# Optimization experiments

Measured on AMD Instinct MI355X. Metric: run time of the kernel, lower is better.

Reference implementation:

```python
import jax, jax.numpy as jnp
import numpy as np


def setup_inputs() -> dict:
    key = jax.random.key(0)
    ks = jax.random.split(key, 5)
    b, t, q_dim, kv_dim, h = 16, 128, 256, 64, 4
    c = t - 1
    q_x = jax.random.normal(ks[0], (b, t, q_dim), dtype=jnp.float32)
    kv_x = jax.random.normal(ks[1], (b, t, c, kv_dim), dtype=jnp.float32)
    # Linear weights stored as [in, out]; no biases (bias=False in torch module).
    sq = 1.0 / np.sqrt(q_dim)
    sk = 1.0 / np.sqrt(kv_dim)
    Wq = jax.random.uniform(ks[2], (q_dim, kv_dim * h), jnp.float32, -sq, sq)
    Wk = jax.random.uniform(ks[3], (kv_dim, kv_dim * h), jnp.float32, -sk, sk)
    Wv = jax.random.uniform(ks[4], (kv_dim, kv_dim * h), jnp.float32, -sk, sk)
    return {"q_x": q_x, "kv_x": kv_x, "Wq": Wq, "Wk": Wk, "Wv": Wv}


def reference(q_x, kv_x, Wq, Wk, Wv):
    b, t, c, k = kv_x.shape  # c = t - 1
    h = Wq.shape[1] // k
    # projections
    q = (q_x @ Wq).reshape(b, t, h, k)          # [b,t,h,k]
    keys = (kv_x @ Wk).reshape(b, t, c, h, k)   # [b,t,c,h,k]
    vals = (kv_x @ Wv).reshape(b, t, c, h, k)
    # per-token attention over the c-sized context
    scores = jnp.einsum('bthk,btchk->bthc', q, keys) / jnp.sqrt(jnp.float32(k))
    w = jax.nn.softmax(scores, axis=-1)          # softmax over context dim
    out = jnp.einsum('bthc,btchk->bthk', w, vals)
    return out.reshape(b, t, h * k)
```

## Files before the change

kernel.cpp:

```cpp
#include <hip/hip_runtime.h>
#include <math.h>

#define Bdim 16
#define Tdim 128
#define Cdim 127
#define Hdim 4
#define QD   256
#define HK   256
#define BT   (Bdim * Tdim)

#define DPP_XOR1 0xB1
#define DPP_XOR2 0x4E
template<int CTRL>
__device__ __forceinline__ float dpp_movf(float x) {
    return __int_as_float(__builtin_amdgcn_update_dpp(
        0, __float_as_int(x), CTRL, 0xF, 0xF, true));
}

__global__ __launch_bounds__(256) void qk_fused(
        const float* __restrict__ q_x,
        const float* __restrict__ Wq,
        const float* __restrict__ Wk,
        float* __restrict__ qk) {
    __shared__ __align__(16) float q_s[4][256];
    __shared__ __align__(16) float p_s[4][4][68];
    int RB = blockIdx.x;
    int tid = threadIdx.x;
    {
        int r = tid >> 6, kq = tid & 63;
        *(float4*)&q_s[r][kq*4] =
            *(const float4*)(q_x + (size_t)(RB*4 + r) * QD + kq * 4);
    }
    __syncthreads();

    float acc[4] = {0.f, 0.f, 0.f, 0.f};
    #pragma unroll 4
    for (int i4 = 0; i4 < 64; ++i4) {
        float w0 = Wq[(size_t)(4*i4+0) * HK + tid];
        float w1 = Wq[(size_t)(4*i4+1) * HK + tid];
        float w2 = Wq[(size_t)(4*i4+2) * HK + tid];
        float w3 = Wq[(size_t)(4*i4+3) * HK + tid];
        #pragma unroll
        for (int r = 0; r < 4; ++r) {
            float4 qv = *(const float4*)&q_s[r][i4*4];
            acc[r] = fmaf(qv.x, w0, fmaf(qv.y, w1, fmaf(qv.z, w2, fmaf(qv.w, w3, acc[r]))));
        }
    }
    int h = tid >> 6, m = tid & 63;
    #pragma unroll
    for (int r = 0; r < 4; ++r) p_s[r][h][m] = acc[r];
    __syncthreads();

    const float4* wk4 = (const float4*)(Wk + (size_t)m * HK + h * 64);
    float4 wkr[16];
    #pragma unroll
    for (int j = 0; j < 16; ++j) wkr[j] = wk4[j];
    float a2[4] = {0.f, 0.f, 0.f, 0.f};
    #pragma unroll
    for (int j4 = 0; j4 < 16; ++j4) {
        #pragma unroll
        for (int r = 0; r < 4; ++r) {
            float4 pv = *(const float4*)&p_s[r][h][j4*4];
            a2[r] = fmaf(pv.x, wkr[j4].x, fmaf(pv.y, wkr[j4].y,
                    fmaf(pv.z, wkr[j4].z, fmaf(pv.w, wkr[j4].w, a2[r]))));
        }
    }
    #pragma unroll
    for (int r = 0; r < 4; ++r)
        qk[(size_t)(RB*4 + r) * HK + tid] = a2[r];
}

__global__ __launch_bounds__(256, 6) void attn_core(
        const float* __restrict__ kv_x,
        const float* __restrict__ qk_g,
        float* __restrict__ wx_buf,
        float* __restrict__ denom_buf) {
    int tid = threadIdx.x;
    int wv = tid >> 6, lane = tid & 63;
    int bt = blockIdx.x * 4 + wv;
    int r  = lane >> 4;
    int g  = (lane >> 2) & 3;
    int jq = lane & 3;
    const float* Xr = kv_x + (size_t)bt * (Cdim * 64);

    const float4* qkp = (const float4*)(qk_g + (size_t)bt * HK + g * 64 + jq * 16);
    float4 Q0 = qkp[0], Q1 = qkp[1], Q2 = qkp[2], Q3 = qkp[3];

    float4 V0 = {0,0,0,0}, V1 = {0,0,0,0}, V2 = {0,0,0,0}, V3 = {0,0,0,0};
    float dsum = 0.f;

    #pragma unroll 2
    for (int k = 0; k < 32; ++k) {
        int c = r + 4 * k;
        bool valid = (c < Cdim);
        const float4* xr = (const float4*)(Xr + (valid ? c : 0) * 64) + jq * 4;
        float4 R0 = xr[0], R1 = xr[1], R2 = xr[2], R3 = xr[3];
        float s;
        s = fmaf(Q0.x, R0.x, Q0.y * R0.y);
        s = fmaf(Q0.z, R0.z, fmaf(Q0.w, R0.w, s));
        s = fmaf(Q1.x, R1.x, fmaf(Q1.y, R1.y, s));
        s = fmaf(Q1.z, R1.z, fmaf(Q1.w, R1.w, s));
        s = fmaf(Q2.x, R2.x, fmaf(Q2.y, R2.y, s));
        s = fmaf(Q2.z, R2.z, fmaf(Q2.w, R2.w, s));
        s = fmaf(Q3.x, R3.x, fmaf(Q3.y, R3.y, s));
        s = fmaf(Q3.z, R3.z, fmaf(Q3.w, R3.w, s));
        s += dpp_movf<DPP_XOR1>(s);
        s += dpp_movf<DPP_XOR2>(s);
        float e = valid ? __expf(s * 0.125f) : 0.f;
        dsum += e;
        V0.x = fmaf(e, R0.x, V0.x); V0.y = fmaf(e, R0.y, V0.y);
        V0.z = fmaf(e, R0.z, V0.z); V0.w = fmaf(e, R0.w, V0.w);
        V1.x = fmaf(e, R1.x, V1.x); V1.y = fmaf(e, R1.y, V1.y);
        V1.z = fmaf(e, R1.z, V1.z); V1.w = fmaf(e, R1.w, V1.w);
        V2.x = fmaf(e, R2.x, V2.x); V2.y = fmaf(e, R2.y, V2.y);
        V2.z = fmaf(e, R2.z, V2.z); V2.w = fmaf(e, R2.w, V2.w);
        V3.x = fmaf(e, R3.x, V3.x); V3.y = fmaf(e, R3.y, V3.y);
        V3.z = fmaf(e, R3.z, V3.z); V3.w = fmaf(e, R3.w, V3.w);
    }

    #pragma unroll
    for (int m = 16; m <= 32; m <<= 1) {
        V0.x += __shfl_xor(V0.x, m, 64); V0.y += __shfl_xor(V0.y, m, 64);
        V0.z += __shfl_xor(V0.z, m, 64); V0.w += __shfl_xor(V0.w, m, 64);
        V1.x += __shfl_xor(V1.x, m, 64); V1.y += __shfl_xor(V1.y, m, 64);
        V1.z += __shfl_xor(V1.z, m, 64); V1.w += __shfl_xor(V1.w, m, 64);
        V2.x += __shfl_xor(V2.x, m, 64); V2.y += __shfl_xor(V2.y, m, 64);
        V2.z += __shfl_xor(V2.z, m, 64); V2.w += __shfl_xor(V2.w, m, 64);
        V3.x += __shfl_xor(V3.x, m, 64); V3.y += __shfl_xor(V3.y, m, 64);
        V3.z += __shfl_xor(V3.z, m, 64); V3.w += __shfl_xor(V3.w, m, 64);
        dsum += __shfl_xor(dsum, m, 64);
    }

    if (r == 0) {
        float4* w = (float4*)(wx_buf + (size_t)bt * HK + g * 64 + jq * 16);
        w[0] = V0; w[1] = V1; w[2] = V2; w[3] = V3;
        if (jq == 0) denom_buf[(size_t)bt * 4 + g] = dsum;
    }
}

__global__ __launch_bounds__(256) void vproj(
        const float* __restrict__ wx_buf,
        const float* __restrict__ denom_buf,
        const float* __restrict__ Wv,
        float* __restrict__ out) {
    __shared__ __align__(16) float4 wx_s[4][64];
    __shared__ __align__(16) float4 dn_s[4];
    int B0 = blockIdx.x * 4;
    int tid = threadIdx.x;
    {
        int r = tid >> 6, l = tid & 63;
        wx_s[r][l] = ((const float4*)(wx_buf + (size_t)(B0 + r) * HK))[l];
    }
    if (tid < 4) dn_s[tid] = *(const float4*)(denom_buf + (size_t)(B0 + tid) * 4);
    __syncthreads();

    int h = tid >> 6;
    float wvr[64];
    #pragma unroll
    for (int j = 0; j < 64; ++j) wvr[j] = Wv[(size_t)j * HK + tid];
    #pragma unroll
    for (int r = 0; r < 4; ++r) {
        float acc = 0.f;
        #pragma unroll
        for (int j4 = 0; j4 < 16; ++j4) {
            float4 w4 = wx_s[r][h * 16 + j4];
            acc = fmaf(w4.x, wvr[j4*4+0], fmaf(w4.y, wvr[j4*4+1],
                  fmaf(w4.z, wvr[j4*4+2], fmaf(w4.w, wvr[j4*4+3], acc))));
        }
        float4 dn = dn_s[r];
        float d = (h == 0) ? dn.x : (h == 1) ? dn.y : (h == 2) ? dn.z : dn.w;
        out[(size_t)(B0 + r) * HK + tid] = acc / d;
    }
}

extern "C" void kernel_launch(void* const* d_in, const int* in_sizes, int n_in,
                              void* d_out, int out_size, void* d_ws, size_t ws_size,
                              hipStream_t stream) {
    const float* q_x  = (const float*)d_in[0];
    const float* kv_x = (const float*)d_in[1];
    const float* Wq   = (const float*)d_in[2];
    const float* Wk   = (const float*)d_in[3];
    const float* Wv   = (const float*)d_in[4];
    float* out = (float*)d_out;

    float* qk    = (float*)d_ws;
    float* wxb   = qk + (size_t)BT * HK;
    float* denom = wxb + (size_t)BT * HK;

    qk_fused <<<BT / 4, 256, 0, stream>>>(q_x, Wq, Wk, qk);
    attn_core<<<BT / 4, 256, 0, stream>>>(kv_x, qk, wxb, denom);
    vproj    <<<BT / 4, 256, 0, stream>>>(wxb, denom, Wv, out);
}
```

Measured before the change: 40.18 us.

## Fuse V projection into attention kernel, split context across four waves per token

The attention core and V-projection kernels are merged into one kernel. Each block now handles a single (b,t) row, with its four waves splitting the 127-long context. Partial weighted sums and denominators are combined through shared memory, and the block then applies Wv and the normalisation directly. This removes one kernel launch and the global round trip of the wx/denominator buffers, and it quadruples the grid size for better latency hiding. The cost is a block-wide sync and per-block Wv reads from global memory without register reuse across rows.

```diff
diff --git a/kernel.cpp b/kernel.cpp
--- a/kernel.cpp
+++ b/kernel.cpp
@@ -70,14 +70,17 @@
         qk[(size_t)(RB*4 + r) * HK + tid] = a2[r];
 }
 
-__global__ __launch_bounds__(256, 6) void attn_core(
+__global__ __launch_bounds__(256, 8) void attn_full(
         const float* __restrict__ kv_x,
         const float* __restrict__ qk_g,
-        float* __restrict__ wx_buf,
-        float* __restrict__ denom_buf) {
+        const float* __restrict__ Wv,
+        float* __restrict__ out) {
+    __shared__ __align__(16) float4 wx_p[4][4][4][4];
+    __shared__ float dn_p[4][4];
+
     int tid = threadIdx.x;
     int wv = tid >> 6, lane = tid & 63;
-    int bt = blockIdx.x * 4 + wv;
+    int bt = blockIdx.x;
     int r  = lane >> 4;
     int g  = (lane >> 2) & 3;
     int jq = lane & 3;
@@ -90,8 +93,8 @@
     float dsum = 0.f;
 
     #pragma unroll 2
-    for (int k = 0; k < 32; ++k) {
-        int c = r + 4 * k;
+    for (int k = 0; k < 8; ++k) {
+        int c = wv * 32 + r + 4 * k;
         bool valid = (c < Cdim);
         const float4* xr = (const float4*)(Xr + (valid ? c : 0) * 64) + jq * 4;
         float4 R0 = xr[0], R1 = xr[1], R2 = xr[2], R3 = xr[3];
@@ -132,44 +135,40 @@
     }
 
     if (r == 0) {
-        float4* w = (float4*)(wx_buf + (size_t)bt * HK + g * 64 + jq * 16);
-        w[0] = V0; w[1] = V1; w[2] = V2; w[3] = V3;
-        if (jq == 0) denom_buf[(size_t)bt * 4 + g] = dsum;
+        wx_p[wv][g][jq][0] = V0;
+        wx_p[wv][g][jq][1] = V1;
+        wx_p[wv][g][jq][2] = V2;
+        wx_p[wv][g][jq][3] = V3;
+        if (jq == 0) dn_p[wv][g] = dsum;
     }
-}
-
-__global__ __launch_bounds__(256) void vproj(
-        const float* __restrict__ wx_buf,
-        const float* __restrict__ denom_buf,
-        const float* __restrict__ Wv,
-        float* __restrict__ out) {
-    __shared__ __align__(16) float4 wx_s[4][64];
-    __shared__ __align__(16) float4 dn_s[4];
-    int B0 = blockIdx.x * 4;
-    int tid = threadIdx.x;
-    {
-        int r = tid >> 6, l = tid & 63;
-        wx_s[r][l] = ((const float4*)(wx_buf + (size_t)(B0 + r) * HK))[l];
-    }
-    if (tid < 4) dn_s[tid] = *(const float4*)(denom_buf + (size_t)(B0 + tid) * 4);
     __syncthreads();
 
-    int h = tid >> 6;
-    float wvr[64];
-    #pragma unroll
-    for (int j = 0; j < 64; ++j) wvr[j] = Wv[(size_t)j * HK + tid];
-    #pragma unroll
-    for (int r = 0; r < 4; ++r) {
+    {
+        int h = tid >> 6, kc = tid & 63;
+        float dn = dn_p[0][h] + dn_p[1][h] + dn_p[2][h] + dn_p[3][h];
+        float inv = 1.f / dn;
+        const float* wvc = Wv + h * 64 + kc;
         float acc = 0.f;
         #pragma unroll
-        for (int j4 = 0; j4 < 16; ++j4) {
-            float4 w4 = wx_s[r][h * 16 + j4];
-            acc = fmaf(w4.x, wvr[j4*4+0], fmaf(w4.y, wvr[j4*4+1],
-                  fmaf(w4.z, wvr[j4*4+2], fmaf(w4.w, wvr[j4*4+3], acc))));
+        for (int q = 0; q < 4; ++q) {
+            #pragma unroll
+            for (int f = 0; f < 4; ++f) {
+                float4 p0 = wx_p[0][h][q][f];
+                float4 p1 = wx_p[1][h][q][f];
+                float4 p2 = wx_p[2][h][q][f];
+                float4 p3 = wx_p[3][h][q][f];
+                float wx0 = p0.x + p1.x + p2.x + p3.x;
+                float wx1 = p0.y + p1.y + p2.y + p3.y;
+                float wx2 = p0.z + p1.z + p2.z + p3.z;
+                float wx3 = p0.w + p1.w + p2.w + p3.w;
+                int j = q * 16 + f * 4;
+                acc = fmaf(wx0, wvc[(size_t)(j+0) * HK],
+                      fmaf(wx1, wvc[(size_t)(j+1) * HK],
+                      fmaf(wx2, wvc[(size_t)(j+2) * HK],
+                      fmaf(wx3, wvc[(size_t)(j+3) * HK], acc))));
+            }
         }
-        float4 dn = dn_s[r];
-        float d = (h == 0) ? dn.x : (h == 1) ? dn.y : (h == 2) ? dn.z : dn.w;
-        out[(size_t)(B0 + r) * HK + tid] = acc / d;
+        out[(size_t)bt * HK + tid] = acc * inv;
     }
 }
 
@@ -183,11 +182,8 @@
     const float* Wv   = (const float*)d_in[4];
     float* out = (float*)d_out;
 
-    float* qk    = (float*)d_ws;
-    float* wxb   = qk + (size_t)BT * HK;
-    float* denom = wxb + (size_t)BT * HK;
+    float* qk = (float*)d_ws;
 
     qk_fused <<<BT / 4, 256, 0, stream>>>(q_x, Wq, Wk, qk);
-    attn_core<<<BT / 4, 256, 0, stream>>>(kv_x, qk, wxb, denom);
-    vproj    <<<BT / 4, 256, 0, stream>>>(wxb, denom, Wv, out);
+    attn_full<<<BT, 256, 0, stream>>>(kv_x, qk, Wv, out);
 }
```

Result: no change. 40.85 us (+1.7%).
